# Performance work log

Measured on AMD Instinct MI355X. Metric: run time of the kernel, lower is better.

## Reference

```python
import jax, jax.numpy as jnp
import numpy as np

K = 2  # top-k experts per token


def setup_inputs() -> dict:
    key = jax.random.key(0)
    k1, k2 = jax.random.split(key)
    B, S, H, E = 4, 4096, 4096, 64
    x = jax.random.normal(k1, (B, S, H), dtype=jnp.float32)
    gate_w = jax.random.normal(k2, (E, H), dtype=jnp.float32) * (H ** -0.5)
    return {"x": x, "gate_w": gate_w}


def reference(x, gate_w):
    # logits = x @ gate_w.T : [B, S, E]
    logits = jnp.einsum("bsh,eh->bse", x, gate_w)
    scores = jax.nn.softmax(logits, axis=-1)
    topk_scores, topk_idx = jax.lax.top_k(scores, K)  # [B, S, K]
    aux_loss = scores.mean() * 0.0
    z_loss = jnp.mean(logits.astype(jnp.float32) ** 2)
    return topk_idx, topk_scores, aux_loss, z_loss
```

## Files before the change

### kernel.cpp

```cpp
#include <hip/hip_runtime.h>
#include <hip/hip_bf16.h>


typedef __bf16  bf16x8  __attribute__((ext_vector_type(8)));
typedef float   f32x16  __attribute__((ext_vector_type(16)));

#define BS_TOK 16384
#define H_DIM  4096
#define E_DIM  64
#define KSPLIT 4
#define KCHUNK (H_DIM / KSPLIT)
#define NPANEL (KCHUNK / 64)
#define WS_ZBUF_OFF (1536u << 10)
#define WS_LG_OFF   (2u << 20)

__device__ __forceinline__ void split3(float v, __bf16 &b0, __bf16 &b1, __bf16 &b2) {
    b0 = (__bf16)v;
    float r = v - (float)b0;
    b1 = (__bf16)r;
    float r2 = r - (float)b1;
    b2 = (__bf16)r2;
}

__device__ __forceinline__ void async_copy16(const float* gp, float* lp) {
    __builtin_amdgcn_global_load_lds(
        (const __attribute__((address_space(1))) void*)gp,
        (__attribute__((address_space(3))) void*)lp, 16, 0, 0);
}

__global__ void prep_w(const float* __restrict__ gw, bf16x8* __restrict__ wb) {
    int idx  = blockIdx.x * blockDim.x + threadIdx.x;
    int kb   = idx >> 7;
    int rem  = idx & 127;
    int nt   = rem >> 6;
    int lane = rem & 63;
    int n  = nt * 32 + (lane & 31);
    int kk = kb * 16 + ((lane >> 5) << 3);
    const float* p = gw + (size_t)n * H_DIM + kk;
    bf16x8 t0, t1, t2;
#pragma unroll
    for (int j = 0; j < 8; ++j) {
        __bf16 a, b, c;
        split3(p[j], a, b, c);
        t0[j] = a; t1[j] = b; t2[j] = c;
    }
    size_t fb = (size_t)(kb * 2 + nt) * 3;
    wb[(fb + 0) * 64 + lane] = t0;
    wb[(fb + 1) * 64 + lane] = t1;
    wb[(fb + 2) * 64 + lane] = t2;
}

__global__ __launch_bounds__(256, 4) void gemm_split(
        const float* __restrict__ x, const bf16x8* __restrict__ wb,
        float* __restrict__ lg) {
    __shared__ float lds[2 * 4096];

    int bid = blockIdx.x;
    int mt  = bid >> 2;
    int kc  = bid & 3;
    int tid = threadIdx.x;
    int w   = tid >> 6;
    int l   = tid & 63;
    int m0  = mt * 64;
    int rw  = (w & 1) * 32;
    int kh  = w >> 1;

    const float* gpan[4];
    int ldso[4];
    int s_slot = l & 15;
#pragma unroll
    for (int r = 0; r < 4; ++r) {
        int g = r * 16 + w * 4 + (l >> 4);
        int c = s_slot ^ (g & 15);
        gpan[r] = x + (size_t)(m0 + g) * H_DIM + kc * KCHUNK + c * 4;
        ldso[r] = (r * 16 + w * 4) * 64;
    }

    f32x16 acc0, acc1;
#pragma unroll
    for (int r = 0; r < 16; ++r) { acc0[r] = 0.f; acc1[r] = 0.f; }

#pragma unroll
    for (int r = 0; r < 4; ++r) async_copy16(gpan[r], &lds[ldso[r]]);

    int row  = rw + (l & 31);
    int half = l >> 5;
    int rsw  = row & 15;

    for (int p = 0; p < NPANEL; ++p) {
        __syncthreads();
        if (p + 1 < NPANEL) {
            int b = (p + 1) & 1;
#pragma unroll
            for (int r = 0; r < 4; ++r)
                async_copy16(gpan[r] + (p + 1) * 64, &lds[b * 4096 + ldso[r]]);
        }
        int bufo = (p & 1) * 4096;
#pragma unroll
        for (int ks2 = 0; ks2 < 2; ++ks2) {
            int ks     = kh * 2 + ks2;
            int ks_abs = kc * 64 + p * 4 + ks;
            int c0     = ks * 4 + half * 2;
            float4 xa = *(const float4*)&lds[bufo + row * 64 + ((c0 ^ rsw) << 2)];
            float4 xb = *(const float4*)&lds[bufo + row * 64 + (((c0 + 1) ^ rsw) << 2)];
            bf16x8 a0, a1, a2;
            float xs[8] = {xa.x, xa.y, xa.z, xa.w, xb.x, xb.y, xb.z, xb.w};
#pragma unroll
            for (int j = 0; j < 8; ++j) {
                __bf16 h0, h1, h2;
                split3(xs[j], h0, h1, h2);
                a0[j] = h0; a1[j] = h1; a2[j] = h2;
            }
            const bf16x8* wp = wb + (size_t)ks_abs * 6 * 64 + l;
            bf16x8 b0 = wp[0*64], b1 = wp[1*64], b2 = wp[2*64];
            bf16x8 b3 = wp[3*64], b4 = wp[4*64], b5 = wp[5*64];
            acc0 = __builtin_amdgcn_mfma_f32_32x32x16_bf16(a0, b0, acc0, 0, 0, 0);
            acc0 = __builtin_amdgcn_mfma_f32_32x32x16_bf16(a1, b0, acc0, 0, 0, 0);
            acc0 = __builtin_amdgcn_mfma_f32_32x32x16_bf16(a2, b0, acc0, 0, 0, 0);
            acc0 = __builtin_amdgcn_mfma_f32_32x32x16_bf16(a0, b1, acc0, 0, 0, 0);
            acc0 = __builtin_amdgcn_mfma_f32_32x32x16_bf16(a1, b1, acc0, 0, 0, 0);
            acc0 = __builtin_amdgcn_mfma_f32_32x32x16_bf16(a0, b2, acc0, 0, 0, 0);
            acc1 = __builtin_amdgcn_mfma_f32_32x32x16_bf16(a0, b3, acc1, 0, 0, 0);
            acc1 = __builtin_amdgcn_mfma_f32_32x32x16_bf16(a1, b3, acc1, 0, 0, 0);
            acc1 = __builtin_amdgcn_mfma_f32_32x32x16_bf16(a2, b3, acc1, 0, 0, 0);
            acc1 = __builtin_amdgcn_mfma_f32_32x32x16_bf16(a0, b4, acc1, 0, 0, 0);
            acc1 = __builtin_amdgcn_mfma_f32_32x32x16_bf16(a1, b4, acc1, 0, 0, 0);
            acc1 = __builtin_amdgcn_mfma_f32_32x32x16_bf16(a0, b5, acc1, 0, 0, 0);
        }
    }

    int col = l & 31;
    if (kh == 1) {
#pragma unroll
        for (int r = 0; r < 16; ++r) {
            int mm = rw + (r & 3) + ((r >> 2) << 3) + (half << 2);
            lds[mm * 64 + col]      = acc0[r];
            lds[mm * 64 + 32 + col] = acc1[r];
        }
    }
    __syncthreads();
    if (kh == 0) {
        size_t obase = (size_t)kc * BS_TOK * E_DIM + (size_t)m0 * E_DIM;
#pragma unroll
        for (int r = 0; r < 16; ++r) {
            int mm = rw + (r & 3) + ((r >> 2) << 3) + (half << 2);
            lg[obase + (size_t)mm * E_DIM + col]
                = acc0[r] + lds[mm * 64 + col];
            lg[obase + (size_t)mm * E_DIM + 32 + col]
                = acc1[r] + lds[mm * 64 + 32 + col];
        }
    }
}

__global__ __launch_bounds__(256) void epilogue(const float* __restrict__ lg,
                                                float* __restrict__ out,
                                                float* __restrict__ zbuf) {
    __shared__ float zsh[4];
    int lane = threadIdx.x & 63;
    int w    = threadIdx.x >> 6;
    int t    = blockIdx.x * 4 + w;

    float l = 0.f;
#pragma unroll
    for (int s = 0; s < KSPLIT; ++s)
        l += lg[((size_t)s * BS_TOK + t) * E_DIM + lane];

    float z = l * l;
#pragma unroll
    for (int off = 32; off; off >>= 1) z += __shfl_xor(z, off);
    if (lane == 0) zsh[w] = z;

    float m = l;
#pragma unroll
    for (int off = 32; off; off >>= 1) m = fmaxf(m, __shfl_xor(m, off));
    float e = expf(l - m);
    float d = e;
#pragma unroll
    for (int off = 32; off; off >>= 1) d += __shfl_xor(d, off);
    float sc = e / d;

    float s1 = sc; int i1 = lane;
#pragma unroll
    for (int off = 32; off; off >>= 1) {
        float os = __shfl_xor(s1, off); int oi = __shfl_xor(i1, off);
        if (os > s1 || (os == s1 && oi < i1)) { s1 = os; i1 = oi; }
    }
    float sm = (lane == i1) ? -1.0f : sc;
    float s2 = sm; int i2 = lane;
#pragma unroll
    for (int off = 32; off; off >>= 1) {
        float os = __shfl_xor(s2, off); int oi = __shfl_xor(i2, off);
        if (os > s2 || (os == s2 && oi < i2)) { s2 = os; i2 = oi; }
    }

    if (lane == 0) {
        out[2 * t]                  = (float)i1;
        out[2 * t + 1]              = (float)i2;
        out[2 * BS_TOK + 2 * t]     = s1;
        out[2 * BS_TOK + 2 * t + 1] = s2;
    }
    __syncthreads();
    if (threadIdx.x == 0)
        zbuf[blockIdx.x] = zsh[0] + zsh[1] + zsh[2] + zsh[3];
}

__global__ __launch_bounds__(256) void zreduce(const float* __restrict__ zbuf,
                                               float* __restrict__ out) {
    __shared__ float sh[4];
    int tid = threadIdx.x;
    float s = 0.f;
#pragma unroll
    for (int i = 0; i < 16; ++i) s += zbuf[tid + 256 * i];
#pragma unroll
    for (int off = 32; off; off >>= 1) s += __shfl_xor(s, off);
    if ((tid & 63) == 0) sh[tid >> 6] = s;
    __syncthreads();
    if (tid == 0) {
        out[4 * BS_TOK]     = 0.0f;
        out[4 * BS_TOK + 1] = (sh[0] + sh[1] + sh[2] + sh[3])
                              * (1.0f / (float)(BS_TOK * E_DIM));
    }
}

extern "C" void kernel_launch(void* const* d_in, const int* in_sizes, int n_in,
                              void* d_out, int out_size, void* d_ws, size_t ws_size,
                              hipStream_t stream) {
    const float* x  = (const float*)d_in[0];
    const float* gw = (const float*)d_in[1];
    float* out  = (float*)d_out;
    bf16x8* wb  = (bf16x8*)d_ws;
    float*  zbf = (float*)((char*)d_ws + WS_ZBUF_OFF);
    float*  lg  = (float*)((char*)d_ws + WS_LG_OFF);

    prep_w<<<128, 256, 0, stream>>>(gw, wb);
    gemm_split<<<(BS_TOK / 64) * KSPLIT, 256, 0, stream>>>(x, wb, lg);
    epilogue<<<BS_TOK / 4, 256, 0, stream>>>(lg, out, zbf);
    zreduce<<<1, 256, 0, stream>>>(zbf, out);
}
```

Baseline: 397.1 us.

## Load x directly into registers with prefetch instead of LDS double-buffering

After: 416.3 us. 4.8% more time.

```diff
diff --git a/kernel.cpp b/kernel.cpp
--- a/kernel.cpp
+++ b/kernel.cpp
@@ -10,7 +10,6 @@
 #define E_DIM  64
 #define KSPLIT 4
 #define KCHUNK (H_DIM / KSPLIT)
-#define NPANEL (KCHUNK / 64)
 #define WS_ZBUF_OFF (1536u << 10)
 #define WS_LG_OFF   (2u << 20)
 
@@ -20,12 +19,6 @@
     b1 = (__bf16)r;
     float r2 = r - (float)b1;
     b2 = (__bf16)r2;
-}
-
-__device__ __forceinline__ void async_copy16(const float* gp, float* lp) {
-    __builtin_amdgcn_global_load_lds(
-        (const __attribute__((address_space(1))) void*)gp,
-        (__attribute__((address_space(3))) void*)lp, 16, 0, 0);
 }
 
 __global__ void prep_w(const float* __restrict__ gw, bf16x8* __restrict__ wb) {
@@ -53,7 +46,7 @@
 __global__ __launch_bounds__(256, 4) void gemm_split(
         const float* __restrict__ x, const bf16x8* __restrict__ wb,
         float* __restrict__ lg) {
-    __shared__ float lds[2 * 4096];
+    __shared__ float red[64 * 64];
 
     int bid = blockIdx.x;
     int mt  = bid >> 2;
@@ -65,68 +58,52 @@
     int rw  = (w & 1) * 32;
     int kh  = w >> 1;
 
-    const float* gpan[4];
-    int ldso[4];
-    int s_slot = l & 15;
-#pragma unroll
-    for (int r = 0; r < 4; ++r) {
-        int g = r * 16 + w * 4 + (l >> 4);
-        int c = s_slot ^ (g & 15);
-        gpan[r] = x + (size_t)(m0 + g) * H_DIM + kc * KCHUNK + c * 4;
-        ldso[r] = (r * 16 + w * 4) * 64;
-    }
-
-    f32x16 acc0, acc1;
-#pragma unroll
-    for (int r = 0; r < 16; ++r) { acc0[r] = 0.f; acc1[r] = 0.f; }
-
-#pragma unroll
-    for (int r = 0; r < 4; ++r) async_copy16(gpan[r], &lds[ldso[r]]);
-
     int row  = rw + (l & 31);
     int half = l >> 5;
-    int rsw  = row & 15;
-
-    for (int p = 0; p < NPANEL; ++p) {
-        __syncthreads();
-        if (p + 1 < NPANEL) {
-            int b = (p + 1) & 1;
-#pragma unroll
-            for (int r = 0; r < 4; ++r)
-                async_copy16(gpan[r] + (p + 1) * 64, &lds[b * 4096 + ldso[r]]);
+
+    const float4* gp = (const float4*)(x + (size_t)(m0 + row) * H_DIM
+                                         + (size_t)(kc * KCHUNK + kh * 512 + half * 8));
+    const bf16x8* wp = wb + (size_t)(kc * 64 + kh * 32) * (6 * 64) + l;
+
+    f32x16 acc0, acc1;
+#pragma unroll
+    for (int r = 0; r < 16; ++r) { acc0[r] = 0.f; acc1[r] = 0.f; }
+
+    float4 pa = gp[0];
+    float4 pb = gp[1];
+
+#pragma unroll 2
+    for (int ks = 0; ks < 32; ++ks) {
+        float4 ca = pa, cb = pb;
+        int nk = (ks + 1) & 31;
+        pa = gp[nk * 4];
+        pb = gp[nk * 4 + 1];
+
+        bf16x8 a0, a1, a2;
+        float xs[8] = {ca.x, ca.y, ca.z, ca.w, cb.x, cb.y, cb.z, cb.w};
+#pragma unroll
+        for (int j = 0; j < 8; ++j) {
+            __bf16 h0, h1, h2;
+            split3(xs[j], h0, h1, h2);
+            a0[j] = h0; a1[j] = h1; a2[j] = h2;
         }
-        int bufo = (p & 1) * 4096;
-#pragma unroll
-        for (int ks2 = 0; ks2 < 2; ++ks2) {
-            int ks     = kh * 2 + ks2;
-            int ks_abs = kc * 64 + p * 4 + ks;
-            int c0     = ks * 4 + half * 2;
-            float4 xa = *(const float4*)&lds[bufo + row * 64 + ((c0 ^ rsw) << 2)];
-            float4 xb = *(const float4*)&lds[bufo + row * 64 + (((c0 + 1) ^ rsw) << 2)];
-            bf16x8 a0, a1, a2;
-            float xs[8] = {xa.x, xa.y, xa.z, xa.w, xb.x, xb.y, xb.z, xb.w};
-#pragma unroll
-            for (int j = 0; j < 8; ++j) {
-                __bf16 h0, h1, h2;
-                split3(xs[j], h0, h1, h2);
-                a0[j] = h0; a1[j] = h1; a2[j] = h2;
-            }
-            const bf16x8* wp = wb + (size_t)ks_abs * 6 * 64 + l;
-            bf16x8 b0 = wp[0*64], b1 = wp[1*64], b2 = wp[2*64];
-            bf16x8 b3 = wp[3*64], b4 = wp[4*64], b5 = wp[5*64];
-            acc0 = __builtin_amdgcn_mfma_f32_32x32x16_bf16(a0, b0, acc0, 0, 0, 0);
-            acc0 = __builtin_amdgcn_mfma_f32_32x32x16_bf16(a1, b0, acc0, 0, 0, 0);
-            acc0 = __builtin_amdgcn_mfma_f32_32x32x16_bf16(a2, b0, acc0, 0, 0, 0);
-            acc0 = __builtin_amdgcn_mfma_f32_32x32x16_bf16(a0, b1, acc0, 0, 0, 0);
-            acc0 = __builtin_amdgcn_mfma_f32_32x32x16_bf16(a1, b1, acc0, 0, 0, 0);
-            acc0 = __builtin_amdgcn_mfma_f32_32x32x16_bf16(a0, b2, acc0, 0, 0, 0);
-            acc1 = __builtin_amdgcn_mfma_f32_32x32x16_bf16(a0, b3, acc1, 0, 0, 0);
-            acc1 = __builtin_amdgcn_mfma_f32_32x32x16_bf16(a1, b3, acc1, 0, 0, 0);
-            acc1 = __builtin_amdgcn_mfma_f32_32x32x16_bf16(a2, b3, acc1, 0, 0, 0);
-            acc1 = __builtin_amdgcn_mfma_f32_32x32x16_bf16(a0, b4, acc1, 0, 0, 0);
-            acc1 = __builtin_amdgcn_mfma_f32_32x32x16_bf16(a1, b4, acc1, 0, 0, 0);
-            acc1 = __builtin_amdgcn_mfma_f32_32x32x16_bf16(a0, b5, acc1, 0, 0, 0);
-        }
+
+        const bf16x8* wq = wp + (size_t)ks * (6 * 64);
+        bf16x8 b0 = wq[0 * 64], b1 = wq[1 * 64], b2 = wq[2 * 64];
+        bf16x8 b3 = wq[3 * 64], b4 = wq[4 * 64], b5 = wq[5 * 64];
+
+        acc0 = __builtin_amdgcn_mfma_f32_32x32x16_bf16(a0, b0, acc0, 0, 0, 0);
+        acc0 = __builtin_amdgcn_mfma_f32_32x32x16_bf16(a1, b0, acc0, 0, 0, 0);
+        acc0 = __builtin_amdgcn_mfma_f32_32x32x16_bf16(a2, b0, acc0, 0, 0, 0);
+        acc0 = __builtin_amdgcn_mfma_f32_32x32x16_bf16(a0, b1, acc0, 0, 0, 0);
+        acc0 = __builtin_amdgcn_mfma_f32_32x32x16_bf16(a1, b1, acc0, 0, 0, 0);
+        acc0 = __builtin_amdgcn_mfma_f32_32x32x16_bf16(a0, b2, acc0, 0, 0, 0);
+        acc1 = __builtin_amdgcn_mfma_f32_32x32x16_bf16(a0, b3, acc1, 0, 0, 0);
+        acc1 = __builtin_amdgcn_mfma_f32_32x32x16_bf16(a1, b3, acc1, 0, 0, 0);
+        acc1 = __builtin_amdgcn_mfma_f32_32x32x16_bf16(a2, b3, acc1, 0, 0, 0);
+        acc1 = __builtin_amdgcn_mfma_f32_32x32x16_bf16(a0, b4, acc1, 0, 0, 0);
+        acc1 = __builtin_amdgcn_mfma_f32_32x32x16_bf16(a1, b4, acc1, 0, 0, 0);
+        acc1 = __builtin_amdgcn_mfma_f32_32x32x16_bf16(a0, b5, acc1, 0, 0, 0);
     }
 
     int col = l & 31;
@@ -134,8 +111,8 @@
 #pragma unroll
         for (int r = 0; r < 16; ++r) {
             int mm = rw + (r & 3) + ((r >> 2) << 3) + (half << 2);
-            lds[mm * 64 + col]      = acc0[r];
-            lds[mm * 64 + 32 + col] = acc1[r];
+            red[mm * 64 + col]      = acc0[r];
+            red[mm * 64 + 32 + col] = acc1[r];
         }
     }
     __syncthreads();
@@ -145,9 +122,9 @@
         for (int r = 0; r < 16; ++r) {
             int mm = rw + (r & 3) + ((r >> 2) << 3) + (half << 2);
             lg[obase + (size_t)mm * E_DIM + col]
-                = acc0[r] + lds[mm * 64 + col];
+                = acc0[r] + red[mm * 64 + col];
             lg[obase + (size_t)mm * E_DIM + 32 + col]
-                = acc1[r] + lds[mm * 64 + 32 + col];
+                = acc1[r] + red[mm * 64 + 32 + col];
         }
     }
 }
```
